# Kernel tuning notes

Measured on AMD Instinct MI355X. Metric: run time of the kernel, lower is better.

The kernel has to match this reference:

```python
import jax, jax.numpy as jnp
import numpy as np
from jax import lax

C = 256          # channels
G = 16           # groups
Cg = C // G      # group channels
K = 3            # kernel size
P = K * K        # sampling points per group
PAD = 1          # spatial padding (dilation=1, stride=1)


def setup_inputs() -> dict:
    key = jax.random.key(0)
    ks = jax.random.split(key, 8)
    def rn(k, shape, s):
        return jax.random.normal(k, shape, dtype=jnp.float32) * s
    N, H, W = 4, 64, 64
    return {
        "x": jax.random.normal(ks[0], (N, C, H, W), dtype=jnp.float32),
        "w_in": rn(ks[1], (C, C), 0.02),
        "b_in": jnp.zeros((C,), jnp.float32),
        "dw_w": rn(ks[2], (C, 1, K, K), 0.1),   # depthwise conv, OIHW with I=1
        "dw_b": jnp.zeros((C,), jnp.float32),
        "ln_g": jnp.ones((C,), jnp.float32),
        "ln_b": jnp.zeros((C,), jnp.float32),
        "w_off": rn(ks[3], (C, G * P * 2), 0.01),
        "b_off": jnp.zeros((G * P * 2,), jnp.float32),
        "w_mask": rn(ks[4], (C, G * P), 0.01),
        "b_mask": jnp.zeros((G * P,), jnp.float32),
        "w_out": rn(ks[5], (C, C), 0.02),
        "b_out": jnp.zeros((C,), jnp.float32),
    }


def _layernorm(x, g, b, eps=1e-5):
    mu = jnp.mean(x, -1, keepdims=True)
    var = jnp.var(x, -1, keepdims=True)
    return (x - mu) * lax.rsqrt(var + eps) * g + b


def _dcnv3_core(xq, offset, mask, offset_scale=1.0):
    # xq: (N, Ho, Wo, C) channels-last value features (matches dcnv3_core_pytorch)
    N, Ho, Wo, _ = xq.shape
    xpad = jnp.pad(xq, ((0, 0), (PAD, PAD), (PAD, PAD), (0, 0)))
    Hi, Wi = Ho + 2 * PAD, Wo + 2 * PAD
    # reference points: pixel centers in padded coords, normalized by (Wi, Hi)
    ry = (jnp.arange(Ho, dtype=jnp.float32) + 0.5 + (K - 1) // 2) / Hi  # (Ho,)
    rx = (jnp.arange(Wo, dtype=jnp.float32) + 0.5 + (K - 1) // 2) / Wi  # (Wo,)
    # dilation grid, kw-major order as in _generate_dilation_grids
    kk = jnp.arange(K, dtype=jnp.float32) - (K - 1) // 2
    gx, gy = jnp.meshgrid(kk, kk, indexing='ij')   # gx over w, gy over h
    gpx = gx.reshape(-1) / Wi                      # (P,)
    gpy = gy.reshape(-1) / Hi
    off = offset.reshape(N, Ho, Wo, G, P, 2)
    # normalized sampling locations, shape (N, Ho, Wo, G, P)
    locx = rx[None, None, :, None, None] + gpx * offset_scale + off[..., 0] * (offset_scale / Wi)
    locy = ry[None, :, None, None, None] + gpy * offset_scale + off[..., 1] * (offset_scale / Hi)
    # grid_sample align_corners=False pixel coords
    px = locx * Wi - 0.5
    py = locy * Hi - 0.5
    x0f = jnp.floor(px); y0f = jnp.floor(py)
    fx = px - x0f; fy = py - y0f
    x0 = x0f.astype(jnp.int32); y0 = y0f.astype(jnp.int32)

    flat = jnp.transpose(xpad.reshape(N, Hi * Wi, G, Cg), (0, 2, 1, 3))  # (N,G,HiWi,Cg)

    def t(a):  # (N,Ho,Wo,G,P) -> (N,G,Ho*Wo,P)
        return jnp.transpose(a.reshape(N, Ho * Wo, G, P), (0, 2, 1, 3))

    def gather(ix, iy):
        valid = (ix >= 0) & (ix < Wi) & (iy >= 0) & (iy < Hi)
        idx = jnp.clip(iy, 0, Hi - 1) * Wi + jnp.clip(ix, 0, Wi - 1)
        idx_t = t(idx).reshape(N, G, Ho * Wo * P, 1)
        v = jnp.take_along_axis(flat, idx_t, axis=2).reshape(N, G, Ho * Wo, P, Cg)
        return v, t(valid).astype(xq.dtype)

    wx1, wy1 = t(fx), t(fy)
    wx0, wy0 = 1.0 - wx1, 1.0 - wy1
    v00, m00 = gather(x0, y0)
    v01, m01 = gather(x0 + 1, y0)
    v10, m10 = gather(x0, y0 + 1)
    v11, m11 = gather(x0 + 1, y0 + 1)
    samp = (v00 * (wx0 * wy0 * m00)[..., None] + v01 * (wx1 * wy0 * m01)[..., None]
            + v10 * (wx0 * wy1 * m10)[..., None] + v11 * (wx1 * wy1 * m11)[..., None])
    mk = t(mask)                                       # (N,G,HoWo,P)
    out = jnp.sum(samp * mk[..., None], axis=3)        # (N,G,HoWo,Cg)
    return jnp.transpose(out, (0, 2, 1, 3)).reshape(N, Ho, Wo, G * Cg)


def reference(x, w_in, b_in, dw_w, dw_b, ln_g, ln_b, w_off, b_off, w_mask, b_mask, w_out, b_out):
    N, _, H, W = x.shape
    x_nhwc = jnp.transpose(x, (0, 2, 3, 1))
    xq = x_nhwc @ w_in + b_in                          # input_proj (value branch)
    # offset/mask branch: depthwise 3x3 conv (channels_first) + LN + GELU
    x1 = lax.conv_general_dilated(x, dw_w, (1, 1), [(PAD, PAD), (PAD, PAD)],
                                  feature_group_count=C,
                                  dimension_numbers=('NCHW', 'OIHW', 'NCHW'))
    x1 = x1 + dw_b[None, :, None, None]
    x1 = jnp.transpose(x1, (0, 2, 3, 1))
    x1 = jax.nn.gelu(_layernorm(x1, ln_g, ln_b), approximate=False)
    offset = x1 @ w_off + b_off                        # (N,H,W,G*P*2)
    mask = x1 @ w_mask + b_mask                        # (N,H,W,G*P)
    mask = jax.nn.softmax(mask.reshape(N, H, W, G, P), axis=-1).reshape(N, H, W, G * P)
    y = _dcnv3_core(xq, offset, mask)
    y = y @ w_out + b_out                              # output_proj
    return jnp.transpose(y, (0, 3, 1, 2))              # back to channels_first
```

## Files before the change

kernel.cpp:

```cpp
#include <hip/hip_runtime.h>
#include <math.h>

#define CCH 256
#define HP2 68
#define WP2 68
#define NPIX 16384

typedef __attribute__((ext_vector_type(8))) short bf16x8;
typedef __attribute__((ext_vector_type(8))) unsigned short u16x8;
typedef __attribute__((ext_vector_type(4))) float f32x4;

__device__ __forceinline__ unsigned short f2bf(float f) {
    unsigned int u = __float_as_uint(f);
    unsigned int r = (u + 0x7fffu + ((u >> 16) & 1u)) >> 16;
    return (unsigned short)r;
}
__device__ __forceinline__ float bf2f(unsigned short h) {
    return __uint_as_float(((unsigned int)h) << 16);
}

__device__ __forceinline__ void gll16(const unsigned short* g, unsigned short* l) {
    __builtin_amdgcn_global_load_lds(
        (const __attribute__((address_space(1))) unsigned int*)g,
        (__attribute__((address_space(3))) unsigned int*)l,
        16, 0, 0);
}

#define OFF_XNBF   0ull
#define OFF_XPAD   8388608ull
#define OFF_X1BF   17858560ull
#define OFF_OFFS   26247168ull
#define OFF_MASK   35684352ull
#define OFF_WTIN   40402944ull
#define OFF_WTOFF  40534016ull
#define OFF_WTMSK  40681472ull
#define OFF_BPAD   40755200ull
#define OFF_WTOUT  40796160ull
#define OFF_BOM    40927232ull
#define OFF_DWT    40928960ull

__global__ __launch_bounds__(256) void prep(const float* __restrict__ x,
                                            unsigned short* __restrict__ xo,
                                            unsigned int* __restrict__ xpadz,
                                            const float* __restrict__ w_in,
                                            const float* __restrict__ w_off,
                                            const float* __restrict__ w_mask,
                                            const float* __restrict__ w_out,
                                            unsigned short* __restrict__ wtin,
                                            unsigned short* __restrict__ wtoff,
                                            unsigned short* __restrict__ wtmsk,
                                            unsigned short* __restrict__ wtout,
                                            const float* __restrict__ b_off,
                                            const float* __restrict__ b_mask,
                                            float* __restrict__ bias_om,
                                            const float* __restrict__ dw_w,
                                            unsigned short* __restrict__ dwtb,
                                            unsigned int* __restrict__ bpad) {
    int z = blockIdx.z;
    int tx = threadIdx.x, ty = threadIdx.y;
    int t = ty * 32 + tx;
    if (z < 4) {
        int flat = (z * 8 + blockIdx.y) * 128 + blockIdx.x;
        unsigned int i = flat * 256 + t;
        if (i < 270336u) {
            int rp = i >> 7, o = i & 127;
            int n = rp / 528, idx = rp % 528;
            int h, w;
            if (idx < 272) {
                static const int hr[4] = {0, 1, 66, 67};
                h = hr[idx / 68]; w = idx % 68;
            } else {
                int j = idx - 272;
                static const int wr[4] = {0, 1, 66, 67};
                h = 2 + (j >> 2); w = wr[j & 3];
            }
            xpadz[(size_t)(n * (HP2 * WP2) + h * WP2 + w) * 128 + o] = 0u;
        }
        __shared__ float tt[32][33];
        int hw0 = blockIdx.x * 32, c0 = blockIdx.y * 32, n = z;
#pragma unroll
        for (int i2 = 0; i2 < 4; i2++)
            tt[ty + i2 * 8][tx] = x[(size_t)(n * CCH + c0 + ty + i2 * 8) * 4096 + hw0 + tx];
        __syncthreads();
#pragma unroll
        for (int i2 = 0; i2 < 4; i2++)
            xo[(size_t)(n * 4096 + hw0 + ty + i2 * 8) * CCH + c0 + tx] = f2bf(tt[tx][ty + i2 * 8]);
        return;
    }
    if (z == 8) {
        if (blockIdx.y == 0) {
            if (blockIdx.x < 2) {
                int i = blockIdx.x * 256 + t;
                if (i < 432) bias_om[i] = (i < 288) ? b_off[i] : b_mask[i - 288];
            } else if (blockIdx.x < 11) {
                int tap = blockIdx.x - 2;
                dwtb[tap * 256 + t] = f2bf(dw_w[t * 9 + tap]);
            } else if (blockIdx.x < 51) {
                bpad[(blockIdx.x - 11) * 256 + t] = 0u;
            }
        }
        return;
    }
    const float* w; unsigned short* wt; int N;
    if (z == 4)      { w = w_in;   wt = wtin;  N = 256; }
    else if (z == 5) { w = w_off;  wt = wtoff; N = 288; }
    else if (z == 6) { w = w_mask; wt = wtmsk; N = 144; }
    else             { w = w_out;  wt = wtout; N = 256; }
    const int K = 256;
    int n0 = blockIdx.x * 32, k0 = blockIdx.y * 32;
    if (n0 >= N) return;
    __shared__ float tb[32][33];
#pragma unroll
    for (int i = 0; i < 4; i++) {
        int k = k0 + ty + i * 8;
        if (n0 + tx < N) tb[ty + i * 8][tx] = w[(size_t)k * N + n0 + tx];
    }
    __syncthreads();
#pragma unroll
    for (int i = 0; i < 4; i++) {
        int n = n0 + ty + i * 8;
        if (n < N) wt[(size_t)n * K + k0 + tx] = f2bf(tb[tx][ty + i * 8]);
    }
}

template<int MODE>
__device__ __forceinline__ void gemm_tile(const unsigned short* __restrict__ A,
                                          const unsigned short* __restrict__ Bt,
                                          const float* __restrict__ bias,
                                          void* __restrict__ C0, void* __restrict__ C1,
                                          int N, int K, int bm, int bn, int tid,
                                          unsigned short* As, unsigned short* Bs) {
    int wid = tid >> 6, lane = tid & 63;
    int wr = wid >> 1, wc = wid & 1;
    int lr = lane & 15, kg = lane >> 4;
    int r = lane >> 2, q = lane & 3;

    const unsigned short* Ag0 = A + (size_t)(bm + 32 * wid + r) * K + q * 8;
    const unsigned short* Ag1 = Ag0 + (size_t)16 * K;
    const unsigned short* Bg0 = Bt + (size_t)(bn + 32 * wid + r) * K + q * 8;
    const unsigned short* Bg1 = Bg0 + (size_t)16 * K;
    unsigned short* Al0 = As + wid * 1024;
    unsigned short* Al1 = Al0 + 512;
    unsigned short* Bl0 = Bs + wid * 1024;
    unsigned short* Bl1 = Bl0 + 512;

    const unsigned short* Ar = As + (wr * 64 + lr) * 32 + kg * 8;
    const unsigned short* Br = Bs + (wc * 64 + lr) * 32 + kg * 8;

    f32x4 acc[4][4];
#pragma unroll
    for (int i = 0; i < 4; i++)
#pragma unroll
        for (int j = 0; j < 4; j++) acc[i][j] = (f32x4){0.f, 0.f, 0.f, 0.f};

    for (int k0 = 0; k0 < K; k0 += 32) {
        gll16(Ag0 + k0, Al0);
        gll16(Ag1 + k0, Al1);
        gll16(Bg0 + k0, Bl0);
        gll16(Bg1 + k0, Bl1);
        __syncthreads();
        bf16x8 a[4], b[4];
#pragma unroll
        for (int i = 0; i < 4; i++) a[i] = *(const bf16x8*)(Ar + i * 512);
#pragma unroll
        for (int j = 0; j < 4; j++) b[j] = *(const bf16x8*)(Br + j * 512);
        __builtin_amdgcn_s_setprio(1);
#pragma unroll
        for (int i = 0; i < 4; i++)
#pragma unroll
            for (int j = 0; j < 4; j++)
                acc[i][j] = __builtin_amdgcn_mfma_f32_16x16x32_bf16(a[i], b[j], acc[i][j], 0, 0, 0);
        __builtin_amdgcn_s_setprio(0);
        __syncthreads();
    }

    int row0 = bm + wr * 64, col0 = bn + wc * 64;
#pragma unroll
    for (int i = 0; i < 4; i++) {
#pragma unroll
        for (int j = 0; j < 4; j++) {
            int col = col0 + j * 16 + lr;
            if (col >= N) continue;
            float bc = (MODE == 4) ? 0.f : bias[col];
#pragma unroll
            for (int r2 = 0; r2 < 4; r2++) {
                int m = row0 + i * 16 + kg * 4 + r2;
                float val = acc[i][j][r2] + bc;
                if (MODE == 1) {
                    int n = m >> 12, hw = m & 4095, h = hw >> 6, w = hw & 63;
                    ((unsigned short*)C0)[(size_t)((n * HP2 + h + 2) * WP2 + (w + 2)) * CCH + col] = f2bf(val);
                } else if (MODE == 4) {
                    int n = col >> 12, hw = col & 4095;
                    ((float*)C0)[(size_t)(n * CCH + m) * 4096 + hw] = val + bias[m];
                } else {
                    if (col < 288)
                        ((unsigned short*)C0)[(size_t)m * 288 + col] = f2bf(val);
                    else
                        ((unsigned short*)C1)[(size_t)m * 144 + (col - 288)] = f2bf(val);
                }
            }
        }
    }
}

template<int MODE>
__global__ __launch_bounds__(256) void gemm_mfma(const unsigned short* __restrict__ A,
                                                 const unsigned short* __restrict__ Bt,
                                                 const float* __restrict__ bias,
                                                 void* __restrict__ C0,
                                                 void* __restrict__ C1,
                                                 int N, int K) {
    __shared__ unsigned short As[4096];
    __shared__ unsigned short Bs[4096];
    gemm_tile<MODE>(A, Bt, bias, C0, C1, N, K, blockIdx.y * 128, blockIdx.x * 128,
                    threadIdx.x, As, Bs);
}

__global__ __launch_bounds__(256) void stage2(const unsigned short* __restrict__ xnbf,
                                              const unsigned short* __restrict__ wtin,
                                              const float* __restrict__ b_in,
                                              unsigned short* __restrict__ xpad,
                                              const unsigned short* __restrict__ dwtb,
                                              const float* __restrict__ dw_b,
                                              const float* __restrict__ ln_g,
                                              const float* __restrict__ ln_b,
                                              unsigned short* __restrict__ x1) {
    __shared__ unsigned short As[4096];
    __shared__ unsigned short Bs[4096];
    int bid = blockIdx.x;
    if (bid < 256) {
        gemm_tile<1>(xnbf, wtin, b_in, xpad, nullptr, 256, 256,
                     (bid >> 1) * 128, (bid & 1) * 128, threadIdx.x, As, Bs);
        return;
    }
    int cb = bid - 256;
    int sb = (cb & 7) * 64 + (cb >> 3);
    int wid = threadIdx.x >> 6, lane = threadIdx.x & 63;
    int sub = lane >> 5, li = lane & 31;
    int mb = sb * 32 + wid * 8 + sub * 4;
    int n = mb >> 12, hw = mb & 4095, h = hw >> 6, w0 = hw & 63;
    int c0 = li << 3;

    float acc[4][8];
    {
        float4 b0 = *(const float4*)(dw_b + c0);
        float4 b1 = *(const float4*)(dw_b + c0 + 4);
        float bb[8] = {b0.x, b0.y, b0.z, b0.w, b1.x, b1.y, b1.z, b1.w};
#pragma unroll
        for (int j = 0; j < 4; j++)
#pragma unroll
            for (int q = 0; q < 8; q++) acc[j][q] = bb[q];
    }
    const u16x8 zz = {0, 0, 0, 0, 0, 0, 0, 0};
#pragma unroll
    for (int ky = 0; ky < 3; ky++) {
        int hy = h + ky - 1;
        if ((unsigned)hy >= 64u) continue;
        const unsigned short* rowp = xnbf + (size_t)(n * 4096 + hy * 64) * CCH + c0;
        u16x8 tap[6];
#pragma unroll
        for (int k6 = 0; k6 < 6; k6++) {
            int wx = w0 + k6 - 1;
            tap[k6] = ((unsigned)wx < 64u) ? *(const u16x8*)(rowp + (size_t)wx * CCH) : zz;
        }
        u16x8 wv[3];
#pragma unroll
        for (int kx = 0; kx < 3; kx++)
            wv[kx] = *(const u16x8*)(dwtb + (ky * 3 + kx) * CCH + c0);
#pragma unroll
        for (int j = 0; j < 4; j++)
#pragma unroll
            for (int kx = 0; kx < 3; kx++)
#pragma unroll
                for (int q = 0; q < 8; q++)
                    acc[j][q] += bf2f(tap[j + kx][q]) * bf2f(wv[kx][q]);
    }
    float s[4], s2[4];
#pragma unroll
    for (int j = 0; j < 4; j++) {
        s[j] = 0.f; s2[j] = 0.f;
#pragma unroll
        for (int q = 0; q < 8; q++) { s[j] += acc[j][q]; s2[j] += acc[j][q] * acc[j][q]; }
    }
#pragma unroll
    for (int off = 16; off; off >>= 1) {
#pragma unroll
        for (int j = 0; j < 4; j++) {
            s[j] += __shfl_xor(s[j], off);
            s2[j] += __shfl_xor(s2[j], off);
        }
    }
    float4 g0 = *(const float4*)(ln_g + c0);
    float4 g1 = *(const float4*)(ln_g + c0 + 4);
    float4 bb0 = *(const float4*)(ln_b + c0);
    float4 bb1 = *(const float4*)(ln_b + c0 + 4);
    float gg[8] = {g0.x, g0.y, g0.z, g0.w, g1.x, g1.y, g1.z, g1.w};
    float bbv[8] = {bb0.x, bb0.y, bb0.z, bb0.w, bb1.x, bb1.y, bb1.z, bb1.w};
    const float is2 = 0.70710678118654752f;
#pragma unroll
    for (int j = 0; j < 4; j++) {
        float mean = s[j] * (1.f / 256.f);
        float var = s2[j] * (1.f / 256.f) - mean * mean;
        float rstd = 1.f / sqrtf(var + 1e-5f);
        u16x8 o;
#pragma unroll
        for (int q = 0; q < 8; q++) {
            float gv = (acc[j][q] - mean) * rstd * gg[q] + bbv[q];
            o[q] = f2bf(0.5f * gv * (1.f + erff(gv * is2)));
        }
        *(u16x8*)(x1 + (size_t)(mb + j) * CCH + c0) = o;
    }
}

__global__ __launch_bounds__(256) void dcn_core(const unsigned short* __restrict__ xpad,
                                                const unsigned short* __restrict__ offs,
                                                const unsigned short* __restrict__ mk,
                                                unsigned short* __restrict__ y) {
    int bid = blockIdx.x;
    int sb = (bid & 7) * 256 + (bid >> 3);
    int t = sb * 256 + threadIdx.x;
    int half = t & 1, g = (t >> 1) & 15, m = t >> 5;
    int n = m >> 12, hw = m & 4095, h = hw >> 6, w = hw & 63;
    const unsigned int* op32 = (const unsigned int*)(offs + (size_t)m * 288 + g * 18);
    const unsigned short* mp = mk + ((size_t)m * 16 + g) * 9;
    const unsigned short* xb = xpad + (size_t)n * (HP2 * WP2 * CCH) + g * 16 + half * 8;

    float mv[9];
    float mx = -1e30f;
#pragma unroll
    for (int i = 0; i < 9; i++) { mv[i] = bf2f(mp[i]); mx = fmaxf(mx, mv[i]); }
    float s = 0.f;
#pragma unroll
    for (int i = 0; i < 9; i++) { mv[i] = expf(mv[i] - mx); s += mv[i]; }
    float rs = 1.f / s;

    float acc[8] = {0.f};
#pragma unroll
    for (int p = 0; p < 9; p++) {
        int dx = p / 3 - 1, dy = p % 3 - 1;
        unsigned int pk = op32[p];
        float ox = bf2f((unsigned short)(pk & 0xffffu));
        float oy = bf2f((unsigned short)(pk >> 16));
        float px = fminf(fmaxf((float)(w + 2 + dx) + ox, 0.f), 67.f);
        float py = fminf(fmaxf((float)(h + 2 + dy) + oy, 0.f), 67.f);
        float x0f = floorf(px), y0f = floorf(py);
        float fx = px - x0f, fy = py - y0f;
        int x0 = (int)x0f, y0 = (int)y0f;
        int x1c = min(x0 + 1, 67), y1c = min(y0 + 1, 67);
        float mval = mv[p] * rs;
        float w00 = (1.f - fx) * (1.f - fy) * mval;
        float w01 = fx * (1.f - fy) * mval;
        float w10 = (1.f - fx) * fy * mval;
        float w11 = fx * fy * mval;
        const unsigned short* r0 = xb + (size_t)y0 * (WP2 * CCH);
        const unsigned short* r1 = xb + (size_t)y1c * (WP2 * CCH);
        u16x8 v00 = *(const u16x8*)(r0 + x0 * CCH);
        u16x8 v01 = *(const u16x8*)(r0 + x1c * CCH);
        u16x8 v10 = *(const u16x8*)(r1 + x0 * CCH);
        u16x8 v11 = *(const u16x8*)(r1 + x1c * CCH);
#pragma unroll
        for (int q = 0; q < 8; q++)
            acc[q] += w00 * bf2f(v00[q]) + w01 * bf2f(v01[q])
                    + w10 * bf2f(v10[q]) + w11 * bf2f(v11[q]);
    }
    u16x8 v;
#pragma unroll
    for (int q = 0; q < 8; q++) v[q] = f2bf(acc[q]);
    *(u16x8*)(y + (size_t)m * CCH + g * 16 + half * 8) = v;
}

extern "C" void kernel_launch(void* const* d_in, const int* in_sizes, int n_in,
                              void* d_out, int out_size, void* d_ws, size_t ws_size,
                              hipStream_t stream) {
    const float* x      = (const float*)d_in[0];
    const float* w_in   = (const float*)d_in[1];
    const float* b_in   = (const float*)d_in[2];
    const float* dw_w   = (const float*)d_in[3];
    const float* dw_b   = (const float*)d_in[4];
    const float* ln_g   = (const float*)d_in[5];
    const float* ln_b   = (const float*)d_in[6];
    const float* w_off  = (const float*)d_in[7];
    const float* b_off  = (const float*)d_in[8];
    const float* w_mask = (const float*)d_in[9];
    const float* b_mask = (const float*)d_in[10];
    const float* w_out  = (const float*)d_in[11];
    const float* b_out  = (const float*)d_in[12];
    float* out = (float*)d_out;
    char* ws = (char*)d_ws;

    unsigned short* xnbf  = (unsigned short*)(ws + OFF_XNBF);
    unsigned short* xpad  = (unsigned short*)(ws + OFF_XPAD);
    unsigned short* x1bf  = (unsigned short*)(ws + OFF_X1BF);
    unsigned short* offs  = (unsigned short*)(ws + OFF_OFFS);
    unsigned short* mkb   = (unsigned short*)(ws + OFF_MASK);
    unsigned short* wtin  = (unsigned short*)(ws + OFF_WTIN);
    unsigned short* wtoff = (unsigned short*)(ws + OFF_WTOFF);
    unsigned short* wtmsk = (unsigned short*)(ws + OFF_WTMSK);
    unsigned int*   bpad  = (unsigned int*)(ws + OFF_BPAD);
    unsigned short* wtout = (unsigned short*)(ws + OFF_WTOUT);
    float*          biasom = (float*)(ws + OFF_BOM);
    unsigned short* dwtb  = (unsigned short*)(ws + OFF_DWT);
    unsigned short* ybf   = xnbf;

    prep<<<dim3(128, 8, 9), dim3(32, 8), 0, stream>>>(x, xnbf, (unsigned int*)xpad,
                                                      w_in, w_off, w_mask, w_out,
                                                      wtin, wtoff, wtmsk, wtout,
                                                      b_off, b_mask, biasom, dw_w, dwtb, bpad);
    stage2<<<768, 256, 0, stream>>>(xnbf, wtin, b_in, xpad, dwtb, dw_b, ln_g, ln_b, x1bf);
    gemm_mfma<5><<<dim3(4, 128), 256, 0, stream>>>(x1bf, wtoff, biasom, offs, mkb, 432, 256);
    dcn_core<<<2048, 256, 0, stream>>>(xpad, offs, mkb, ybf);
    gemm_mfma<4><<<dim3(128, 2), 256, 0, stream>>>(wtout, ybf, b_out, out, nullptr, 16384, 256);
}
```

Measured before the change: 77.76 us.

## Use group-planar padded value layout and packed per-group offset/mask records

Changes the padded value tensor from channels-last to per-(batch,group) planes of 16 channels, so the bilinear corner loads of neighbouring pixels are contiguous. The offset and mask GEMM now writes a 32-element record per (group,pixel), holding 18 offsets and 9 mask logits, which the DCN core reads with four vector loads. Thread mapping in the core is reordered so consecutive threads cover consecutive pixels within a group, improving locality of gathers. The cost is scattered, non-coalesced stores in the GEMM epilogues (division by 18 and 9, strided 16-element writes) and a larger workspace.

```diff
diff --git a/kernel.cpp b/kernel.cpp
--- a/kernel.cpp
+++ b/kernel.cpp
@@ -4,6 +4,7 @@
 #define CCH 256
 #define HP2 68
 #define WP2 68
+#define PLANE 4624
 #define NPIX 16384
 
 typedef __attribute__((ext_vector_type(8))) short bf16x8;
@@ -29,15 +30,14 @@
 #define OFF_XNBF   0ull
 #define OFF_XPAD   8388608ull
 #define OFF_X1BF   17858560ull
-#define OFF_OFFS   26247168ull
-#define OFF_MASK   35684352ull
-#define OFF_WTIN   40402944ull
-#define OFF_WTOFF  40534016ull
-#define OFF_WTMSK  40681472ull
-#define OFF_BPAD   40755200ull
-#define OFF_WTOUT  40796160ull
-#define OFF_BOM    40927232ull
-#define OFF_DWT    40928960ull
+#define OFF_REC    26247168ull
+#define OFF_WTIN   43024384ull
+#define OFF_WTOFF  43155456ull
+#define OFF_WTMSK  43302912ull
+#define OFF_BPAD   43376640ull
+#define OFF_WTOUT  43417600ull
+#define OFF_BOM    43548672ull
+#define OFF_DWT    43550400ull
 
 __global__ __launch_bounds__(256) void prep(const float* __restrict__ x,
                                             unsigned short* __restrict__ xo,
@@ -63,8 +63,10 @@
         int flat = (z * 8 + blockIdx.y) * 128 + blockIdx.x;
         unsigned int i = flat * 256 + t;
         if (i < 270336u) {
-            int rp = i >> 7, o = i & 127;
-            int n = rp / 528, idx = rp % 528;
+            int o = i & 7;
+            int rp = i >> 3;
+            int n = rp / 8448, rem = rp % 8448;
+            int g = rem / 528, idx = rem % 528;
             int h, w;
             if (idx < 272) {
                 static const int hr[4] = {0, 1, 66, 67};
@@ -74,7 +76,7 @@
                 static const int wr[4] = {0, 1, 66, 67};
                 h = 2 + (j >> 2); w = wr[j & 3];
             }
-            xpadz[(size_t)(n * (HP2 * WP2) + h * WP2 + w) * 128 + o] = 0u;
+            xpadz[((size_t)(n * 16 + g) * PLANE + h * WP2 + w) * 8 + o] = 0u;
         }
         __shared__ float tt[32][33];
         int hw0 = blockIdx.x * 32, c0 = blockIdx.y * 32, n = z;
@@ -127,7 +129,7 @@
 __device__ __forceinline__ void gemm_tile(const unsigned short* __restrict__ A,
                                           const unsigned short* __restrict__ Bt,
                                           const float* __restrict__ bias,
-                                          void* __restrict__ C0, void* __restrict__ C1,
+                                          void* __restrict__ C0,
                                           int N, int K, int bm, int bn, int tid,
                                           unsigned short* As, unsigned short* Bs) {
     int wid = tid >> 6, lane = tid & 63;
@@ -188,15 +190,16 @@
                 float val = acc[i][j][r2] + bc;
                 if (MODE == 1) {
                     int n = m >> 12, hw = m & 4095, h = hw >> 6, w = hw & 63;
-                    ((unsigned short*)C0)[(size_t)((n * HP2 + h + 2) * WP2 + (w + 2)) * CCH + col] = f2bf(val);
+                    int g = col >> 4, c = col & 15;
+                    ((unsigned short*)C0)[((size_t)(n * 16 + g) * PLANE + (h + 2) * WP2 + (w + 2)) * 16 + c] = f2bf(val);
                 } else if (MODE == 4) {
                     int n = col >> 12, hw = col & 4095;
                     ((float*)C0)[(size_t)(n * CCH + m) * 4096 + hw] = val + bias[m];
                 } else {
-                    if (col < 288)
-                        ((unsigned short*)C0)[(size_t)m * 288 + col] = f2bf(val);
-                    else
-                        ((unsigned short*)C1)[(size_t)m * 144 + (col - 288)] = f2bf(val);
+                    int g, j2;
+                    if (col < 288) { g = col / 18; j2 = col % 18; }
+                    else { int cc = col - 288; g = cc / 9; j2 = 18 + cc % 9; }
+                    ((unsigned short*)C0)[((size_t)g * NPIX + m) * 32 + j2] = f2bf(val);
                 }
             }
         }
@@ -208,11 +211,10 @@
                                                  const unsigned short* __restrict__ Bt,
                                                  const float* __restrict__ bias,
                                                  void* __restrict__ C0,
-                                                 void* __restrict__ C1,
                                                  int N, int K) {
     __shared__ unsigned short As[4096];
     __shared__ unsigned short Bs[4096];
-    gemm_tile<MODE>(A, Bt, bias, C0, C1, N, K, blockIdx.y * 128, blockIdx.x * 128,
+    gemm_tile<MODE>(A, Bt, bias, C0, N, K, blockIdx.y * 128, blockIdx.x * 128,
                     threadIdx.x, As, Bs);
 }
 
@@ -229,7 +231,7 @@
     __shared__ unsigned short Bs[4096];
     int bid = blockIdx.x;
     if (bid < 256) {
-        gemm_tile<1>(xnbf, wtin, b_in, xpad, nullptr, 256, 256,
+        gemm_tile<1>(xnbf, wtin, b_in, xpad, 256, 256,
                      (bid >> 1) * 128, (bid & 1) * 128, threadIdx.x, As, Bs);
         return;
     }
@@ -313,51 +315,63 @@
 }
 
 __global__ __launch_bounds__(256) void dcn_core(const unsigned short* __restrict__ xpad,
-                                                const unsigned short* __restrict__ offs,
-                                                const unsigned short* __restrict__ mk,
+                                                const unsigned short* __restrict__ recs,
                                                 unsigned short* __restrict__ y) {
     int bid = blockIdx.x;
     int sb = (bid & 7) * 256 + (bid >> 3);
-    int t = sb * 256 + threadIdx.x;
-    int half = t & 1, g = (t >> 1) & 15, m = t >> 5;
+    int u = sb * 256 + threadIdx.x;
+    int half = u & 1;
+    int w32 = (u >> 1) & 31;
+    int rest = u >> 6;
+    int g = rest & 15;
+    int mb = rest >> 4;
+    int m = mb * 32 + w32;
     int n = m >> 12, hw = m & 4095, h = hw >> 6, w = hw & 63;
-    const unsigned int* op32 = (const unsigned int*)(offs + (size_t)m * 288 + g * 18);
-    const unsigned short* mp = mk + ((size_t)m * 16 + g) * 9;
-    const unsigned short* xb = xpad + (size_t)n * (HP2 * WP2 * CCH) + g * 16 + half * 8;
+
+    const unsigned short* rec = recs + ((size_t)g * NPIX + m) * 32;
+    u16x8 L0 = *(const u16x8*)(rec);
+    u16x8 L1 = *(const u16x8*)(rec + 8);
+    u16x8 L2 = *(const u16x8*)(rec + 16);
+    u16x8 L3 = *(const u16x8*)(rec + 24);
+    unsigned short ctl[27];
+#pragma unroll
+    for (int e = 0; e < 8; e++) { ctl[e] = L0[e]; ctl[8 + e] = L1[e]; ctl[16 + e] = L2[e]; }
+    ctl[24] = L3[0]; ctl[25] = L3[1]; ctl[26] = L3[2];
 
     float mv[9];
     float mx = -1e30f;
 #pragma unroll
-    for (int i = 0; i < 9; i++) { mv[i] = bf2f(mp[i]); mx = fmaxf(mx, mv[i]); }
+    for (int i = 0; i < 9; i++) { mv[i] = bf2f(ctl[18 + i]); mx = fmaxf(mx, mv[i]); }
     float s = 0.f;
 #pragma unroll
     for (int i = 0; i < 9; i++) { mv[i] = expf(mv[i] - mx); s += mv[i]; }
     float rs = 1.f / s;
 
+    const unsigned short* xb = xpad + (size_t)(n * 16 + g) * (PLANE * 16) + half * 8;
+
     float acc[8] = {0.f};
 #pragma unroll
     for (int p = 0; p < 9; p++) {
         int dx = p / 3 - 1, dy = p % 3 - 1;
-        unsigned int pk = op32[p];
-        float ox = bf2f((unsigned short)(pk & 0xffffu));
-        float oy = bf2f((unsigned short)(pk >> 16));
+        float ox = bf2f(ctl[2 * p]);
+        float oy = bf2f(ctl[2 * p + 1]);
         float px = fminf(fmaxf((float)(w + 2 + dx) + ox, 0.f), 67.f);
         float py = fminf(fmaxf((float)(h + 2 + dy) + oy, 0.f), 67.f);
         float x0f = floorf(px), y0f = floorf(py);
         float fx = px - x0f, fy = py - y0f;
         int x0 = (int)x0f, y0 = (int)y0f;
-        int x1c = min(x0 + 1, 67), y1c = min(y0 + 1, 67);
+        int y1c = min(y0 + 1, 67);
         float mval = mv[p] * rs;
         float w00 = (1.f - fx) * (1.f - fy) * mval;
         float w01 = fx * (1.f - fy) * mval;
         float w10 = (1.f - fx) * fy * mval;
         float w11 = fx * fy * mval;
-        const unsigned short* r0 = xb + (size_t)y0 * (WP2 * CCH);
-        const unsigned short* r1 = xb + (size_t)y1c * (WP2 * CCH);
-        u16x8 v00 = *(const u16x8*)(r0 + x0 * CCH);
-        u16x8 v01 = *(const u16x8*)(r0 + x1c * CCH);
-        u16x8 v10 = *(const u16x8*)(r1 + x0 * CCH);
-        u16x8 v11 = *(const u16x8*)(r1 + x1c * CCH);
+        const unsigned short* r0 = xb + ((size_t)y0 * WP2 + x0) * 16;
+        const unsigned short* r1 = xb + ((size_t)y1c * WP2 + x0) * 16;
+        u16x8 v00 = *(const u16x8*)(r0);
+        u16x8 v01 = *(const u16x8*)(r0 + 16);
+        u16x8 v10 = *(const u16x8*)(r1);
+        u16x8 v11 = *(const u16x8*)(r1 + 16);
 #pragma unroll
         for (int q = 0; q < 8; q++)
             acc[q] += w00 * bf2f(v00[q]) + w01 * bf2f(v01[q])
@@ -391,8 +405,7 @@
     unsigned short* xnbf  = (unsigned short*)(ws + OFF_XNBF);
     unsigned short* xpad  = (unsigned short*)(ws + OFF_XPAD);
     unsigned short* x1bf  = (unsigned short*)(ws + OFF_X1BF);
-    unsigned short* offs  = (unsigned short*)(ws + OFF_OFFS);
-    unsigned short* mkb   = (unsigned short*)(ws + OFF_MASK);
+    unsigned short* recs  = (unsigned short*)(ws + OFF_REC);
     unsigned short* wtin  = (unsigned short*)(ws + OFF_WTIN);
     unsigned short* wtoff = (unsigned short*)(ws + OFF_WTOFF);
     unsigned short* wtmsk = (unsigned short*)(ws + OFF_WTMSK);
@@ -407,7 +420,7 @@
                                                       wtin, wtoff, wtmsk, wtout,
                                                       b_off, b_mask, biasom, dw_w, dwtb, bpad);
     stage2<<<768, 256, 0, stream>>>(xnbf, wtin, b_in, xpad, dwtb, dw_b, ln_g, ln_b, x1bf);
-    gemm_mfma<5><<<dim3(4, 128), 256, 0, stream>>>(x1bf, wtoff, biasom, offs, mkb, 432, 256);
-    dcn_core<<<2048, 256, 0, stream>>>(xpad, offs, mkb, ybf);
-    gemm_mfma<4><<<dim3(128, 2), 256, 0, stream>>>(wtout, ybf, b_out, out, nullptr, 16384, 256);
-}
+    gemm_mfma<5><<<dim3(4, 128), 256, 0, stream>>>(x1bf, wtoff, biasom, recs, 432, 256);
+    dcn_core<<<2048, 256, 0, stream>>>(xpad, recs, ybf);
+    gemm_mfma<4><<<dim3(128, 2), 256, 0, stream>>>(wtout, ybf, b_out, out, 16384, 256);
+}
```

Result: no change. 78.90 us (+1.5%).
